# Optimization experiments

Measured on AMD Instinct MI355X. Metric: run time of the kernel, lower is better.

Reference implementation:

```python
import jax, jax.numpy as jnp
import numpy as np
from jax import lax

CONF_THRES = 0.25
IOU_THRES = 0.45
MAX_WH = 4096.0   # class offset, agnostic=False
MAX_DET = 300
NEG = jnp.float32(-1e30)


def setup_inputs() -> dict:
    key = jax.random.key(0)
    B, N, C = 16, 25200, 85  # 640x640 yolov5, nc=80
    k1, k2, k3, k4 = jax.random.split(key, 4)
    xy = jax.random.uniform(k1, (B, N, 2), jnp.float32, 0.0, 640.0)
    wh = jax.random.uniform(k2, (B, N, 2), jnp.float32, 4.0, 120.0)
    obj = jax.random.uniform(k3, (B, N, 1), jnp.float32)
    cls = jax.random.uniform(k4, (B, N, C - 5), jnp.float32)
    prediction = jnp.concatenate([xy, wh, obj, cls], axis=-1)
    return {"prediction": prediction}


def _xywh2xyxy(b):
    # b: [N,4] (cx,cy,w,h) -> (x1,y1,x2,y2)
    return jnp.concatenate([b[:, :2] - b[:, 2:4] * 0.5,
                            b[:, :2] + b[:, 2:4] * 0.5], axis=1)


def _iou_one_vs_all(box, boxes):
    # box: [4], boxes: [N,4], plain IoU as in torchvision.ops.nms
    x1 = jnp.maximum(box[0], boxes[:, 0])
    y1 = jnp.maximum(box[1], boxes[:, 1])
    x2 = jnp.minimum(box[2], boxes[:, 2])
    y2 = jnp.minimum(box[3], boxes[:, 3])
    inter = jnp.clip(x2 - x1, 0.0) * jnp.clip(y2 - y1, 0.0)
    a1 = (box[2] - box[0]) * (box[3] - box[1])
    a2 = (boxes[:, 2] - boxes[:, 0]) * (boxes[:, 3] - boxes[:, 1])
    return inter / (a1 + a2 - inter)


def _nms_image(p):
    # p: [N, 5+nc] single-image predictions (decoded xywh, obj, class scores)
    obj = p[:, 4]                               # [N]
    cls_scores = p[:, 5:] * obj[:, None]        # x[:,5:] *= x[:,4:5]
    conf = jnp.max(cls_scores, axis=1)          # best-class conf
    j = jnp.argmax(cls_scores, axis=1)          # best class id
    boxes = _xywh2xyxy(p[:, :4])                # [N,4]
    valid = (obj > CONF_THRES) & (conf > CONF_THRES)
    # class-offset boxes for per-class NMS (agnostic=False)
    nms_boxes = boxes + (j.astype(boxes.dtype) * MAX_WH)[:, None]

    s0 = jnp.where(valid, conf, NEG)

    def step(s_live, _):
        i = jnp.argmax(s_live)
        sel = s_live[i]
        keep = sel > 0.0
        iou = _iou_one_vs_all(nms_boxes[i], nms_boxes)
        suppress = keep & (iou > IOU_THRES)
        s_new = jnp.where(suppress, NEG, s_live).at[i].set(NEG)
        return s_new, (i, keep)

    _, (idxs, keeps) = lax.scan(step, s0, None, length=MAX_DET)
    # output rows [x1,y1,x2,y2,conf,cls] — boxes WITHOUT class offset
    rows = jnp.concatenate([boxes[idxs], conf[idxs, None],
                            j[idxs, None].astype(boxes.dtype)], axis=1)
    rows = rows * keeps[:, None].astype(rows.dtype)  # zero padded slots
    return rows, keeps


def reference(prediction):
    # prediction: [B, N, 5+nc] -> ([B, MAX_DET, 6], [B, MAX_DET] keep mask)
    out, keep = jax.vmap(_nms_image)(prediction)
    return out, keep
```

## Files before the change

kernel.cpp:

```cpp
#include <hip/hip_runtime.h>
#include <cstdint>
#include <cfloat>

#define BATCH 16
#define NBOX 25200
#define CH 85
#define NCLS 80
#define CAP 512
#define SEGCAP 128
#define ACC 32
#define MAXDET 300
#define RPB 112
#define CNTPAD 16

typedef unsigned long long u64;

__device__ __forceinline__ u64 shflx64(u64 v, int m) {
    int lo = __shfl_xor((int)(unsigned)(v & 0xffffffffu), m);
    int hi = __shfl_xor((int)(unsigned)(v >> 32), m);
    return ((u64)(unsigned)hi << 32) | (u64)(unsigned)lo;
}

__global__ __launch_bounds__(256) void pre_kernel(const float* __restrict__ p,
                                                  int* __restrict__ cnt,
                                                  u64* __restrict__ rec,
                                                  float* __restrict__ outZero,
                                                  int outN) {
#pragma clang fp contract(off)
    __shared__ float s[RPB * CH];
    int tid = threadIdx.x;

    long z = (long)blockIdx.x * 256 + tid;
    if (z < outN) outZero[z] = 0.0f;

    long blockRow = (long)blockIdx.x * RPB;

    const float4* p4 = (const float4*)(p + blockRow * CH);
    float4* s4 = (float4*)s;
    for (int t = tid; t < RPB * CH / 4; t += 256) {
        __builtin_amdgcn_global_load_lds(
            (const __attribute__((address_space(1))) void*)(p4 + t),
            (__attribute__((address_space(3))) void*)(s4 + (t & ~63)),
            16, 0, 0);
    }
    __syncthreads();

    int r = tid >> 1;
    int half = tid & 1;
    if (r < RPB) {
        const float* row = s + r * CH;
        float obj = row[4];

        float v = -FLT_MAX; int c = 1000;
        int c0 = half * 40;
        for (int k = 0; k < 40; k++) {
            float sc = row[5 + c0 + k] * obj;
            int cc = c0 + k;
            if (sc > v) { v = sc; c = cc; }
        }
        float v2 = __shfl_xor(v, 1);
        int   cz = __shfl_xor(c, 1);
        if (v2 > v || (v2 == v && cz < c)) { v = v2; c = cz; }

        if (half == 0 && obj > 0.25f && v > 0.25f) {
            int wid = (int)blockRow + r;
            int b   = wid / NBOX;
            int idx = wid - b * NBOX;
            u64 key = ((u64)__float_as_uint(v) << 22) | ((u64)(32767 - idx) << 7) | (u64)c;
            int bkt = b * NCLS + c;
            int seg = idx & 3;
            int pos = atomicAdd(&cnt[bkt * CNTPAD + seg], 1);
            if (pos < SEGCAP) {
                float x = row[0], y = row[1], w = row[2], h = row[3];
                float hw = w * 0.5f, hh = h * 0.5f;
                float offc = (float)c * 4096.0f;
                float4 b4;
                b4.x = (x - hw) + offc; b4.y = (y - hh) + offc;
                b4.z = (x + hw) + offc; b4.w = (y + hh) + offc;
                u64* slot = rec + ((long)bkt * CAP + seg * SEGCAP + pos) * 4;
                *(float4*)slot = b4;
                slot[2] = key;
            }
        }
    }
}

__global__ __launch_bounds__(64) void nms_kernel(const int* __restrict__ cnt,
                                                 const u64* __restrict__ rec,
                                                 u64* __restrict__ accKey) {
#pragma clang fp contract(off)
    __shared__ float4 posBox[CAP];
    __shared__ u64    posKeyS[CAP];
    __shared__ u64    rowLds[64];
    __shared__ int    pickPosLds[ACC];
    int lane = threadIdx.x;
    int bkt = blockIdx.x;

    const int* cb = cnt + bkt * CNTPAD;
    int ns0 = cb[0], ns1 = cb[1], ns2 = cb[2], ns3 = cb[3];
    ns0 = ns0 < SEGCAP ? ns0 : SEGCAP;
    ns1 = ns1 < SEGCAP ? ns1 : SEGCAP;
    ns2 = ns2 < SEGCAP ? ns2 : SEGCAP;
    ns3 = ns3 < SEGCAP ? ns3 : SEGCAP;
    int nsg[4] = {ns0, ns1, ns2, ns3};
    int ntot = ns0 + ns1 + ns2 + ns3;

    const u64* R = rec + (long)bkt * CAP * 4;
    u64 key[8];
#pragma unroll
    for (int r = 0; r < 8; r++) {
        int slot = (r << 6) | lane;
        float4 b4 = *(const float4*)(R + (long)slot * 4);
        u64 k = R[(long)slot * 4 + 2];
        posBox[slot] = b4;
        int off = ((r & 1) << 6) | lane;
        key[r] = (off < nsg[r >> 1]) ? ((k << 9) | (u64)slot) : 0ULL;
    }
    __syncthreads();

#define CE_XL(K, LM)                                                    \
    { bool d = ((lane & ((K) >> 3)) == 0);                              \
      _Pragma("unroll")                                                 \
      for (int r = 0; r < 8; r++) {                                     \
          u64 part = shflx64(key[r], (LM));                             \
          bool up = ((lane & (LM)) == 0);                               \
          bool gt = key[r] > part;                                      \
          u64 mx = gt ? key[r] : part;                                  \
          u64 mn = gt ? part : key[r];                                  \
          key[r] = (d == up) ? mx : mn; } }
#define CE_RR(K, M)                                                    \
    { _Pragma("unroll")                                                \
      for (int r = 0; r < 8; r++) if (!(r & (M))) {                    \
          int r2 = r | (M);                                            \
          u64 a = key[r], e = key[r2];                                 \
          bool d = ((r & (K)) == 0);                                   \
          u64 hi = (a > e) ? a : e, lo = (a > e) ? e : a;              \
          key[r]  = d ? hi : lo;                                       \
          key[r2] = d ? lo : hi; } }
#define CE_RL(K, M)                                                    \
    { bool d = ((lane & ((K) >> 3)) == 0);                             \
      _Pragma("unroll")                                                \
      for (int r = 0; r < 8; r++) if (!(r & (M))) {                    \
          int r2 = r | (M);                                            \
          u64 a = key[r], e = key[r2];                                 \
          u64 hi = (a > e) ? a : e, lo = (a > e) ? e : a;              \
          key[r]  = d ? hi : lo;                                       \
          key[r2] = d ? lo : hi; } }

    CE_RR(2, 1)
    CE_RR(4, 2) CE_RR(4, 1)
    CE_RL(8, 4) CE_RL(8, 2) CE_RL(8, 1)
    CE_XL(16, 1)  CE_RL(16, 4)  CE_RL(16, 2)  CE_RL(16, 1)
    CE_XL(32, 2)  CE_XL(32, 1)  CE_RL(32, 4)  CE_RL(32, 2)  CE_RL(32, 1)
    CE_XL(64, 4)  CE_XL(64, 2)  CE_XL(64, 1)  CE_RL(64, 4)  CE_RL(64, 2)  CE_RL(64, 1)
    CE_XL(128, 8) CE_XL(128, 4) CE_XL(128, 2) CE_XL(128, 1)
    CE_RL(128, 4) CE_RL(128, 2) CE_RL(128, 1)
    CE_XL(256, 16) CE_XL(256, 8) CE_XL(256, 4) CE_XL(256, 2) CE_XL(256, 1)
    CE_RL(256, 4)  CE_RL(256, 2) CE_RL(256, 1)
    CE_XL(512, 32) CE_XL(512, 16) CE_XL(512, 8) CE_XL(512, 4) CE_XL(512, 2) CE_XL(512, 1)
    CE_RL(512, 4)  CE_RL(512, 2)  CE_RL(512, 1)
#undef CE_XL
#undef CE_RR
#undef CE_RL

    float4 pb[8]; u64 pk[8];
#pragma unroll
    for (int r = 0; r < 8; r++) {
        int slot = (int)(key[r] & 511u);
        pb[r] = posBox[slot];
        pk[r] = key[r] >> 9;
    }
    __syncthreads();
#pragma unroll
    for (int r = 0; r < 8; r++) {
        int t = (lane << 3) | r;
        posBox[t]  = pb[r];
        posKeyS[t] = pk[r];
    }
    __syncthreads();

    long obase = (long)bkt * ACC;
    int nacc = 0;
    for (int tb = 0; tb < CAP; tb += 64) {
        if (tb >= ntot || nacc >= ACC) break;
        if (tb > 0) __syncthreads();

        bool valid = (tb + lane) < ntot;
        float4 my = posBox[tb + lane];
        float myA = (my.z - my.x) * (my.w - my.y);
        bool dead = !valid;

        if (tb > 0) {
            for (int k = 0; k < nacc; k++) {
                float4 B = posBox[pickPosLds[k]];
                float xx1 = fmaxf(B.x, my.x);
                float yy1 = fmaxf(B.y, my.y);
                float xx2 = fminf(B.z, my.z);
                float yy2 = fminf(B.w, my.w);
                float inter = fmaxf(xx2 - xx1, 0.0f) * fmaxf(yy2 - yy1, 0.0f);
                float A = (B.z - B.x) * (B.w - B.y);
                float uni = (A + myA) - inter;
                if (valid && (inter / uni > 0.45f)) dead = true;
            }
        }

        u64 row = 0;
#pragma unroll 4
        for (int k = 1; k < 64; k++) {
            int j = (lane + k) & 63;
            float4 B = posBox[tb + j];
            float xx1 = fmaxf(my.x, B.x);
            float yy1 = fmaxf(my.y, B.y);
            float xx2 = fminf(my.z, B.z);
            float yy2 = fminf(my.w, B.w);
            float inter = fmaxf(xx2 - xx1, 0.0f) * fmaxf(yy2 - yy1, 0.0f);
            float aj = (B.z - B.x) * (B.w - B.y);
            float uni = (myA + aj) - inter;
            if (inter / uni > 0.45f) row |= 1ULL << j;
        }

        u64 alive = __ballot(!dead);
        rowLds[lane] = row;
        __syncthreads();

        while (alive != 0ULL && nacc < ACC) {
            int pos = (int)__ffsll((long long)alive) - 1;
            if (lane == 0) {
                accKey[obase + nacc] = posKeyS[tb + pos];
                pickPosLds[nacc] = tb + pos;
            }
            nacc++;
            u64 krow = rowLds[pos];
            alive &= ~krow;
            alive &= ~(1ULL << pos);
        }
    }

    for (int t2 = nacc + lane; t2 < ACC; t2 += 64) accKey[obase + t2] = 0ULL;
}

__global__ __launch_bounds__(256) void merge_kernel(const float* __restrict__ p,
                                                    const u64* __restrict__ accKey,
                                                    float* __restrict__ outRows,
                                                    float* __restrict__ outKeep) {
#pragma clang fp contract(off)
    __shared__ u64 L[NCLS * ACC];
    int tid = threadIdx.x;
    int b = blockIdx.y;
    const u64* src = accKey + (long)b * NCLS * ACC;
    for (int t = tid; t < NCLS * ACC; t += 256) L[t] = src[t];
    __syncthreads();

    int g = blockIdx.x * 256 + tid;
    u64 key = L[g];
    if (key == 0ULL) return;
    int cOwn = g / ACC;
    int rank = g - cOwn * ACC;

    int d = 1;
    for (; d + 3 < NCLS; d += 4) {
        int ca = cOwn + d;     if (ca >= NCLS) ca -= NCLS;
        int cb = cOwn + d + 1; if (cb >= NCLS) cb -= NCLS;
        int cc = cOwn + d + 2; if (cc >= NCLS) cc -= NCLS;
        int cd = cOwn + d + 3; if (cd >= NCLS) cd -= NCLS;
        const u64* LA = L + ca * ACC;
        const u64* LB = L + cb * ACC;
        const u64* LC = L + cc * ACC;
        const u64* LD = L + cd * ACC;
        int na = 0, nb = 0, nc = 0, nd = 0;
#pragma unroll
        for (int s2 = 32; s2; s2 >>= 1) {
            int ta = na + s2, tb2 = nb + s2, tc = nc + s2, td = nd + s2;
            if (ta <= ACC && LA[ta - 1] > key) na = ta;
            if (tb2 <= ACC && LB[tb2 - 1] > key) nb = tb2;
            if (tc <= ACC && LC[tc - 1] > key) nc = tc;
            if (td <= ACC && LD[td - 1] > key) nd = td;
        }
        rank += na + nb + nc + nd;
        if (rank >= MAXDET) return;
    }
    for (; d < NCLS; d++) {
        int c2 = cOwn + d; if (c2 >= NCLS) c2 -= NCLS;
        const u64* Lc = L + c2 * ACC;
        int cn = 0;
#pragma unroll
        for (int s2 = 32; s2; s2 >>= 1) {
            int ncx = cn + s2;
            if (ncx <= ACC && Lc[ncx - 1] > key) cn = ncx;
        }
        rank += cn;
        if (rank >= MAXDET) return;
    }

    int cc  = (int)(key & 127);
    int idx = 32767 - (int)((key >> 7) & 32767);
    float conf = __uint_as_float((unsigned)(key >> 22));
    const float* q = p + ((long)b * NBOX + idx) * CH;
    float x = q[0], y = q[1], w = q[2], h = q[3];
    float hw = w * 0.5f, hh = h * 0.5f;
    float* row = outRows + ((long)b * MAXDET + rank) * 6;
    row[0] = x - hw; row[1] = y - hh; row[2] = x + hw; row[3] = y + hh;
    row[4] = conf;   row[5] = (float)cc;
    outKeep[b * MAXDET + rank] = 1.0f;
}

extern "C" void kernel_launch(void* const* d_in, const int* in_sizes, int n_in,
                              void* d_out, int out_size, void* d_ws, size_t ws_size,
                              hipStream_t stream) {
    const float* p = (const float*)d_in[0];
    float* out = (float*)d_out;

    char* ws = (char*)d_ws;
    int* cnt = (int*)ws;
    u64* rec = (u64*)(ws + BATCH * NCLS * CNTPAD * 4);
    u64* accKey = (u64*)(ws + BATCH * NCLS * CNTPAD * 4
                            + (size_t)BATCH * NCLS * CAP * 32);

    hipMemsetAsync(cnt, 0, BATCH * NCLS * CNTPAD * sizeof(int), stream);
    pre_kernel<<<(BATCH * NBOX) / RPB, 256, 0, stream>>>(p, cnt, rec, out, out_size);
    nms_kernel<<<BATCH * NCLS, 64, 0, stream>>>(cnt, rec, accKey);
    dim3 gM(NCLS * ACC / 256, BATCH);
    merge_kernel<<<gM, 256, 0, stream>>>(p, accKey, out, out + (size_t)BATCH * MAXDET * 6);
}
```

Baseline: 262.8 us.

## Use 256-thread shared-memory bitonic sort in NMS kernel and halve rows per block

```diff
diff --git a/kernel.cpp b/kernel.cpp
--- a/kernel.cpp
+++ b/kernel.cpp
@@ -10,16 +10,10 @@
 #define SEGCAP 128
 #define ACC 32
 #define MAXDET 300
-#define RPB 112
+#define RPB 56
 #define CNTPAD 16
 
 typedef unsigned long long u64;
-
-__device__ __forceinline__ u64 shflx64(u64 v, int m) {
-    int lo = __shfl_xor((int)(unsigned)(v & 0xffffffffu), m);
-    int hi = __shfl_xor((int)(unsigned)(v >> 32), m);
-    return ((u64)(unsigned)hi << 32) | (u64)(unsigned)lo;
-}
 
 __global__ __launch_bounds__(256) void pre_kernel(const float* __restrict__ p,
                                                   int* __restrict__ cnt,
@@ -85,15 +79,17 @@
     }
 }
 
-__global__ __launch_bounds__(64) void nms_kernel(const int* __restrict__ cnt,
-                                                 const u64* __restrict__ rec,
-                                                 u64* __restrict__ accKey) {
+__global__ __launch_bounds__(256) void nms_kernel(const int* __restrict__ cnt,
+                                                  const u64* __restrict__ rec,
+                                                  u64* __restrict__ accKey) {
 #pragma clang fp contract(off)
-    __shared__ float4 posBox[CAP];
-    __shared__ u64    posKeyS[CAP];
+    __shared__ float4 boxSlot[CAP];
+    __shared__ u64    keyArr[CAP];
+    __shared__ float4 boxRank[CAP];
     __shared__ u64    rowLds[64];
     __shared__ int    pickPosLds[ACC];
-    int lane = threadIdx.x;
+    __shared__ int    naccLds;
+    int tid = threadIdx.x;
     int bkt = blockIdx.x;
 
     const int* cb = cnt + bkt * CNTPAD;
@@ -106,137 +102,101 @@
     int ntot = ns0 + ns1 + ns2 + ns3;
 
     const u64* R = rec + (long)bkt * CAP * 4;
-    u64 key[8];
-#pragma unroll
-    for (int r = 0; r < 8; r++) {
-        int slot = (r << 6) | lane;
-        float4 b4 = *(const float4*)(R + (long)slot * 4);
-        u64 k = R[(long)slot * 4 + 2];
-        posBox[slot] = b4;
-        int off = ((r & 1) << 6) | lane;
-        key[r] = (off < nsg[r >> 1]) ? ((k << 9) | (u64)slot) : 0ULL;
-    }
-    __syncthreads();
-
-#define CE_XL(K, LM)                                                    \
-    { bool d = ((lane & ((K) >> 3)) == 0);                              \
-      _Pragma("unroll")                                                 \
-      for (int r = 0; r < 8; r++) {                                     \
-          u64 part = shflx64(key[r], (LM));                             \
-          bool up = ((lane & (LM)) == 0);                               \
-          bool gt = key[r] > part;                                      \
-          u64 mx = gt ? key[r] : part;                                  \
-          u64 mn = gt ? part : key[r];                                  \
-          key[r] = (d == up) ? mx : mn; } }
-#define CE_RR(K, M)                                                    \
-    { _Pragma("unroll")                                                \
-      for (int r = 0; r < 8; r++) if (!(r & (M))) {                    \
-          int r2 = r | (M);                                            \
-          u64 a = key[r], e = key[r2];                                 \
-          bool d = ((r & (K)) == 0);                                   \
-          u64 hi = (a > e) ? a : e, lo = (a > e) ? e : a;              \
-          key[r]  = d ? hi : lo;                                       \
-          key[r2] = d ? lo : hi; } }
-#define CE_RL(K, M)                                                    \
-    { bool d = ((lane & ((K) >> 3)) == 0);                             \
-      _Pragma("unroll")                                                \
-      for (int r = 0; r < 8; r++) if (!(r & (M))) {                    \
-          int r2 = r | (M);                                            \
-          u64 a = key[r], e = key[r2];                                 \
-          u64 hi = (a > e) ? a : e, lo = (a > e) ? e : a;              \
-          key[r]  = d ? hi : lo;                                       \
-          key[r2] = d ? lo : hi; } }
-
-    CE_RR(2, 1)
-    CE_RR(4, 2) CE_RR(4, 1)
-    CE_RL(8, 4) CE_RL(8, 2) CE_RL(8, 1)
-    CE_XL(16, 1)  CE_RL(16, 4)  CE_RL(16, 2)  CE_RL(16, 1)
-    CE_XL(32, 2)  CE_XL(32, 1)  CE_RL(32, 4)  CE_RL(32, 2)  CE_RL(32, 1)
-    CE_XL(64, 4)  CE_XL(64, 2)  CE_XL(64, 1)  CE_RL(64, 4)  CE_RL(64, 2)  CE_RL(64, 1)
-    CE_XL(128, 8) CE_XL(128, 4) CE_XL(128, 2) CE_XL(128, 1)
-    CE_RL(128, 4) CE_RL(128, 2) CE_RL(128, 1)
-    CE_XL(256, 16) CE_XL(256, 8) CE_XL(256, 4) CE_XL(256, 2) CE_XL(256, 1)
-    CE_RL(256, 4)  CE_RL(256, 2) CE_RL(256, 1)
-    CE_XL(512, 32) CE_XL(512, 16) CE_XL(512, 8) CE_XL(512, 4) CE_XL(512, 2) CE_XL(512, 1)
-    CE_RL(512, 4)  CE_RL(512, 2)  CE_RL(512, 1)
-#undef CE_XL
-#undef CE_RR
-#undef CE_RL
-
-    float4 pb[8]; u64 pk[8];
-#pragma unroll
-    for (int r = 0; r < 8; r++) {
-        int slot = (int)(key[r] & 511u);
-        pb[r] = posBox[slot];
-        pk[r] = key[r] >> 9;
-    }
-    __syncthreads();
-#pragma unroll
-    for (int r = 0; r < 8; r++) {
-        int t = (lane << 3) | r;
-        posBox[t]  = pb[r];
-        posKeyS[t] = pk[r];
-    }
+    for (int s = tid; s < CAP; s += 256) {
+        float4 b4 = *(const float4*)(R + (long)s * 4);
+        u64 k = R[(long)s * 4 + 2];
+        boxSlot[s] = b4;
+        int seg = s >> 7, off = s & 127;
+        keyArr[s] = (off < nsg[seg]) ? ((k << 9) | (u64)s) : 0ULL;
+    }
+    __syncthreads();
+
+    for (int K = 2; K <= CAP; K <<= 1) {
+        for (int J = K >> 1; J >= 1; J >>= 1) {
+            int i = (tid << 1) - (tid & (J - 1));
+            bool desc = ((i & K) == 0);
+            u64 a = keyArr[i], b = keyArr[i + J];
+            bool sw = desc ? (a < b) : (a > b);
+            if (sw) { keyArr[i] = b; keyArr[i + J] = a; }
+            __syncthreads();
+        }
+    }
+
+    for (int s = tid; s < CAP; s += 256) {
+        u64 tk = keyArr[s];
+        boxRank[s] = boxSlot[(int)(tk & 511u)];
+        keyArr[s] = tk >> 9;
+    }
+    if (tid == 0) naccLds = 0;
     __syncthreads();
 
     long obase = (long)bkt * ACC;
-    int nacc = 0;
     for (int tb = 0; tb < CAP; tb += 64) {
-        if (tb >= ntot || nacc >= ACC) break;
-        if (tb > 0) __syncthreads();
-
-        bool valid = (tb + lane) < ntot;
-        float4 my = posBox[tb + lane];
-        float myA = (my.z - my.x) * (my.w - my.y);
-        bool dead = !valid;
-
-        if (tb > 0) {
-            for (int k = 0; k < nacc; k++) {
-                float4 B = posBox[pickPosLds[k]];
-                float xx1 = fmaxf(B.x, my.x);
-                float yy1 = fmaxf(B.y, my.y);
-                float xx2 = fminf(B.z, my.z);
-                float yy2 = fminf(B.w, my.w);
+        int nacc0 = naccLds;
+        if (tb >= ntot || nacc0 >= ACC) break;
+
+        bool dead = true;
+        float4 my = make_float4(0.f, 0.f, 0.f, 0.f);
+        if (tid < 64) {
+            bool valid = (tb + tid) < ntot;
+            my = boxRank[tb + tid];
+            float myA = (my.z - my.x) * (my.w - my.y);
+            dead = !valid;
+
+            if (tb > 0) {
+                for (int k = 0; k < nacc0; k++) {
+                    float4 B = boxRank[pickPosLds[k]];
+                    float xx1 = fmaxf(B.x, my.x);
+                    float yy1 = fmaxf(B.y, my.y);
+                    float xx2 = fminf(B.z, my.z);
+                    float yy2 = fminf(B.w, my.w);
+                    float inter = fmaxf(xx2 - xx1, 0.0f) * fmaxf(yy2 - yy1, 0.0f);
+                    float A = (B.z - B.x) * (B.w - B.y);
+                    float uni = (A + myA) - inter;
+                    if (valid && (inter / uni > 0.45f)) dead = true;
+                }
+            }
+
+            u64 row = 0;
+#pragma unroll 4
+            for (int k = 1; k < 64; k++) {
+                int j = (tid + k) & 63;
+                float4 B = boxRank[tb + j];
+                float xx1 = fmaxf(my.x, B.x);
+                float yy1 = fmaxf(my.y, B.y);
+                float xx2 = fminf(my.z, B.z);
+                float yy2 = fminf(my.w, B.w);
                 float inter = fmaxf(xx2 - xx1, 0.0f) * fmaxf(yy2 - yy1, 0.0f);
-                float A = (B.z - B.x) * (B.w - B.y);
-                float uni = (A + myA) - inter;
-                if (valid && (inter / uni > 0.45f)) dead = true;
-            }
-        }
-
-        u64 row = 0;
-#pragma unroll 4
-        for (int k = 1; k < 64; k++) {
-            int j = (lane + k) & 63;
-            float4 B = posBox[tb + j];
-            float xx1 = fmaxf(my.x, B.x);
-            float yy1 = fmaxf(my.y, B.y);
-            float xx2 = fminf(my.z, B.z);
-            float yy2 = fminf(my.w, B.w);
-            float inter = fmaxf(xx2 - xx1, 0.0f) * fmaxf(yy2 - yy1, 0.0f);
-            float aj = (B.z - B.x) * (B.w - B.y);
-            float uni = (myA + aj) - inter;
-            if (inter / uni > 0.45f) row |= 1ULL << j;
-        }
-
-        u64 alive = __ballot(!dead);
-        rowLds[lane] = row;
+                float aj = (B.z - B.x) * (B.w - B.y);
+                float uni = (myA + aj) - inter;
+                if (inter / uni > 0.45f) row |= 1ULL << j;
+            }
+            rowLds[tid] = row;
+        }
         __syncthreads();
 
-        while (alive != 0ULL && nacc < ACC) {
-            int pos = (int)__ffsll((long long)alive) - 1;
-            if (lane == 0) {
-                accKey[obase + nacc] = posKeyS[tb + pos];
-                pickPosLds[nacc] = tb + pos;
-            }
-            nacc++;
-            u64 krow = rowLds[pos];
-            alive &= ~krow;
-            alive &= ~(1ULL << pos);
-        }
-    }
-
-    for (int t2 = nacc + lane; t2 < ACC; t2 += 64) accKey[obase + t2] = 0ULL;
+        if (tid < 64) {
+            u64 alive = __ballot(!dead);
+            int nacc = nacc0;
+            while (alive != 0ULL && nacc < ACC) {
+                int pos = (int)__ffsll((long long)alive) - 1;
+                if (tid == 0) {
+                    accKey[obase + nacc] = keyArr[tb + pos];
+                    pickPosLds[nacc] = tb + pos;
+                }
+                nacc++;
+                u64 krow = rowLds[pos];
+                alive &= ~krow;
+                alive &= ~(1ULL << pos);
+            }
+            if (tid == 0) naccLds = nacc;
+        }
+        __syncthreads();
+    }
+
+    __syncthreads();
+    int fn = naccLds;
+    for (int t2 = fn + tid; t2 < ACC; t2 += 256) accKey[obase + t2] = 0ULL;
 }
 
 __global__ __launch_bounds__(256) void merge_kernel(const float* __restrict__ p,
@@ -318,7 +278,7 @@
 
     hipMemsetAsync(cnt, 0, BATCH * NCLS * CNTPAD * sizeof(int), stream);
     pre_kernel<<<(BATCH * NBOX) / RPB, 256, 0, stream>>>(p, cnt, rec, out, out_size);
-    nms_kernel<<<BATCH * NCLS, 64, 0, stream>>>(cnt, rec, accKey);
+    nms_kernel<<<BATCH * NCLS, 256, 0, stream>>>(cnt, rec, accKey);
     dim3 gM(NCLS * ACC / 256, BATCH);
     merge_kernel<<<gM, 256, 0, stream>>>(p, accKey, out, out + (size_t)BATCH * MAXDET * 6);
 }
```

New measurement: 257.0 us. -2.2%, faster.
